# Kernel optimization log

Hardware: AMD Instinct MI355X
Metric: run time of the kernel (lower is better)

The kernel has to match this reference:

```python
import jax, jax.numpy as jnp
import numpy as np

# Static config (matches init_kwargs)
B, C, H, W = 16, 3, 64, 64
K = 32            # num_kernels
D = 5             # tree_depth
S = 1 << D        # leaves per tree = 32
R = 5             # receptive_field_size
STRIDE, PAD = 1, 0
TAU = 1.0
OH = (H + 2 * PAD - R) // STRIDE + 1
OW = (W + 2 * PAD - R) // STRIDE + 1
P = OH * OW       # number of output spatial positions

# LUT[op, t] = truth-table value of 2-input logic op `op` at minterm t = 2*a + b
LUT = jnp.asarray(np.array([[(op >> t) & 1 for t in range(4)]
                            for op in range(16)], dtype=np.float32))


def _combine(a, b, w):
    """Differentiable LUT node: softmax-weighted mixture of all 16 binary ops.
    a, b: (B, K, P, N) child activations; w: (N, K, 16) logits."""
    p = jax.nn.softmax(w / TAU, axis=-1)          # (N, K, 16)
    v = jnp.einsum('nko,ot->nkt', p, LUT)         # (N, K, 4) minterm coeffs
    c = jnp.transpose(v, (1, 0, 2))[None, :, None]  # (1, K, 1, N, 4)
    return (c[..., 0] * (1 - a) * (1 - b)
            + c[..., 1] * (1 - a) * b
            + c[..., 2] * a * (1 - b)
            + c[..., 3] * a * b)


def setup_inputs() -> dict:
    key = jax.random.key(0)
    ks = jax.random.split(key, 10)
    x = jax.random.uniform(ks[0], (B, C, H, W), dtype=jnp.float32)
    h_idx = jax.random.randint(ks[1], (2, K, S), 0, R, dtype=jnp.int32)
    w_idx = jax.random.randint(ks[2], (2, K, S), 0, R, dtype=jnp.int32)
    c_idx = jax.random.randint(ks[3], (2, K, S), 0, C, dtype=jnp.int32)
    node_counts = [S >> lvl for lvl in range(D + 1)]  # [32,16,8,4,2,1]
    ws = {f'w{i}': jax.random.normal(ks[4 + i], (n, K, 16), dtype=jnp.float32)
          for i, n in enumerate(node_counts)}
    return {'x': x, 'h_idx': h_idx, 'w_idx': w_idx, 'c_idx': c_idx, **ws}


def reference(x, h_idx, w_idx, c_idx, w0, w1, w2, w3, w4, w5):
    if PAD > 0:
        x = jnp.pad(x, ((0, 0), (0, 0), (PAD, PAD), (PAD, PAD)))
    # Absolute gather indices: leaf offsets + strided window origins
    off_h = jnp.repeat(jnp.arange(OH, dtype=jnp.int32) * STRIDE, OW)  # (P,)
    off_w = jnp.tile(jnp.arange(OW, dtype=jnp.int32) * STRIDE, OH)    # (P,)
    Habs = h_idx[:, :, None, :] + off_h[None, None, :, None]  # (2,K,P,S)
    Wabs = w_idx[:, :, None, :] + off_w[None, None, :, None]  # (2,K,P,S)
    Cabs = jnp.broadcast_to(c_idx[:, :, None, :], Habs.shape)  # (2,K,P,S)
    g = x[:, Cabs, Habs, Wabs]                                 # (B,2,K,P,S)

    # Level 0: combine the two gathered leaf inputs per node
    y = _combine(g[:, 0], g[:, 1], w0)                         # (B,K,P,S)
    # Levels 1..D: pair consecutive nodes and reduce up the binary tree
    for w in (w1, w2, w3, w4, w5):
        y = _combine(y[..., 0::2], y[..., 1::2], w)
    return y.reshape(y.shape[0], K, OH, OW)
```

## Files before the change

### kernel.cpp

```cpp
#include <hip/hip_runtime.h>
#include <hip/hip_fp16.h>
#include <math.h>

#define Bb   16
#define Cc   3
#define Hh   64
#define Ww   64
#define Kk   32
#define Ss   32
#define OHh  60
#define OWw  60
#define Pp   3600
#define ROWS 34
#define OHSUB 30
#define NGRP 450
#define TPB  256

#define DWROW  33
#define DWC    (ROWS * DWROW)
#define DWCOPY (Cc * DWC)

typedef float vf4 __attribute__((ext_vector_type(4)));
typedef float vf4u __attribute__((ext_vector_type(4), aligned(4)));

#define SB __builtin_amdgcn_sched_barrier(0)

static __device__ __forceinline__ vf4 vsplat(float s) { return (vf4){s, s, s, s}; }

static __device__ __forceinline__ vf4 comb(vf4 a, vf4 b, vf4 c) {
    const vf4 t = __builtin_elementwise_fma(b, vsplat(c.w), vsplat(c.y));
    const vf4 u = __builtin_elementwise_fma(b, vsplat(c.z), vsplat(c.x));
    return __builtin_elementwise_fma(a, t, u);
}

static __device__ __forceinline__ unsigned int pkh(float lo, float hi) {
    __half2 h = __floats2half2_rn(lo, hi);
    return *reinterpret_cast<unsigned int*>(&h);
}

#define GATH(dbase, dst)                                                     \
    {                                                                        \
        const unsigned int lo = xsh[(dbase) + loff];                         \
        const unsigned int hi = xsh[(dbase) + loff + 1];                     \
        const __half2 hl = *reinterpret_cast<const __half2*>(&lo);           \
        const __half2 hh = *reinterpret_cast<const __half2*>(&hi);           \
        const float2 fl = __half22float2(hl);                                \
        const float2 fh = __half22float2(hh);                                \
        dst = (vf4){fl.x, fl.y, fh.x, fh.y};                                 \
    }

#define STAGE(S, LASTQ, FOLD_DS, FOLD_FMA)                                    \
    vf4 t4_##S;                                                               \
    {                                                                         \
        vf4 A0, B0, A1, B1, A2, B2, A3, B3;                                   \
        GATH(cb0.x, A0); GATH(cb0.y, B0);                                     \
        GATH(cb1.x, A1); GATH(cb1.y, B1);                                     \
        GATH(cb2.x, A2); GATH(cb2.y, B2);                                     \
        GATH(cb3.x, A3); GATH(cb3.y, B3);                                     \
        const vf4 c0 = coefs[4*S], c1 = coefs[4*S+1];                         \
        const vf4 c2 = coefs[4*S+2], c3 = coefs[4*S+3];                       \
        const vf4 d0 = coefs[32+2*S], d1 = coefs[33+2*S], e0 = coefs[48+S];   \
        FOLD_DS                                                               \
        if constexpr (!(LASTQ)) {                                             \
            cb0 = bases[(4*S+4) & 31]; cb1 = bases[(4*S+5) & 31];             \
            cb2 = bases[(4*S+6) & 31]; cb3 = bases[(4*S+7) & 31];             \
        }                                                                     \
        const vf4 u0 = comb(A0, B0, c0), u1 = comb(A1, B1, c1);               \
        const vf4 u2 = comb(A2, B2, c2), u3 = comb(A3, B3, c3);               \
        t4_##S = comb(comb(u0, u1, d0), comb(u2, u3, d1), e0);                \
        FOLD_FMA                                                              \
        SB;                                                                   \
    }

__global__ __launch_bounds__(TPB) void logic_conv_kernel(
    const float* __restrict__ x,
    const int*   __restrict__ h_idx,
    const int*   __restrict__ w_idx,
    const int*   __restrict__ c_idx,
    const float* __restrict__ w0, const float* __restrict__ w1,
    const float* __restrict__ w2, const float* __restrict__ w3,
    const float* __restrict__ w4, const float* __restrict__ w5,
    float* __restrict__ out)
{
    __shared__ unsigned int xsh[2 * DWCOPY];
    __shared__ vf4  coefs[63];
    __shared__ int2 bases[32];

    const int tid  = threadIdx.x;
    const int blk  = blockIdx.x;
    const int b    = blk >> 6;
    const int k    = (blk >> 1) & 31;
    const int half = blk & 1;
    const int oh0  = half * OHSUB;

    const float* xb = x + b * (Cc * Hh * Ww);
    #pragma unroll
    for (int it = 0; it < 7; ++it) {
        const int flat = it * TPB + tid;
        if (flat < Cc * ROWS * 16) {
            const int c   = flat / (ROWS * 16);
            const int rem = flat - c * (ROWS * 16);
            const int r   = rem >> 4;
            const int w4i = rem & 15;
            const int w0c = w4i << 2;
            const float* src = xb + c * (Hh * Ww) + (oh0 + r) * Ww + w0c;
            const vf4u A = *reinterpret_cast<const vf4u*>(src);
            vf4u Bv;
            if (w4i < 15) Bv = *reinterpret_cast<const vf4u*>(src + 1);
            else          Bv = (vf4u){A.y, A.z, A.w, A.w};
            const int di = c * DWC + r * DWROW + (w0c >> 1);
            xsh[di]              = pkh(A.x, A.y);
            xsh[di + 1]          = pkh(A.z, A.w);
            xsh[DWCOPY + di]     = pkh(Bv.x, Bv.y);
            xsh[DWCOPY + di + 1] = pkh(Bv.z, Bv.w);
        }
    }

    if (tid < 32) {
        const int i0 = (0 * Kk + k) * Ss + tid;
        const int i1 = (1 * Kk + k) * Ss + tid;
        const int wA = w_idx[i0], sA = wA & 1;
        const int wB = w_idx[i1], sB = wB & 1;
        bases[tid] = make_int2(
            sA * DWCOPY + c_idx[i0] * DWC + h_idx[i0] * DWROW + ((wA - sA) >> 1),
            sB * DWCOPY + c_idx[i1] * DWC + h_idx[i1] * DWROW + ((wB - sB) >> 1));
    }

    if (tid >= 64 && tid < 127) {
        const int t = tid - 64;
        const float* wp; int n;
        if      (t < 32) { wp = w0; n = t;      }
        else if (t < 48) { wp = w1; n = t - 32; }
        else if (t < 56) { wp = w2; n = t - 48; }
        else if (t < 60) { wp = w3; n = t - 56; }
        else if (t < 62) { wp = w4; n = t - 60; }
        else             { wp = w5; n = 0;      }
        const float* lg = wp + (n * Kk + k) * 16;
        float l[16];
        float m = lg[0];
        #pragma unroll
        for (int q = 0; q < 16; ++q) { l[q] = lg[q]; m = fmaxf(m, l[q]); }
        float e[16], s = 0.f;
        #pragma unroll
        for (int q = 0; q < 16; ++q) { e[q] = __expf(l[q] - m); s += e[q]; }
        const float inv = 1.f / s;
        float c0 = 0.f, c1 = 0.f, c2 = 0.f, c3 = 0.f;
        #pragma unroll
        for (int op = 0; op < 16; ++op) {
            if (op & 1) c0 += e[op];
            if (op & 2) c1 += e[op];
            if (op & 4) c2 += e[op];
            if (op & 8) c3 += e[op];
        }
        c0 *= inv; c1 *= inv; c2 *= inv; c3 *= inv;
        coefs[t] = (vf4){c0, c2 - c0, c1 - c0, c0 - c1 - c2 + c3};
    }

    __syncthreads();

    float* outp = out + (b * Kk + k) * Pp + oh0 * OWw;
    #pragma unroll 1
    for (int it = 0; it < 2; ++it) {
        const int g = it * TPB + tid;
        if (g < NGRP) {
            const int oh   = g % OHSUB;
            const int owg  = g / OHSUB;
            const int loff = oh * DWROW + (owg << 1);

            int2 cb0 = bases[0], cb1 = bases[1], cb2 = bases[2], cb3 = bases[3];
            vf4 t8a, t8b, t16a, t16b, y;

            STAGE(0, 0, , )
            STAGE(1, 0,
                  const vf4 f0 = coefs[56];,
                  t8a = comb(t4_0, t4_1, f0);)
            STAGE(2, 0, , )
            STAGE(3, 0,
                  const vf4 f1 = coefs[57]; const vf4 g0 = coefs[60];,
                  t8b = comb(t4_2, t4_3, f1); t16a = comb(t8a, t8b, g0);)
            STAGE(4, 0, , )
            STAGE(5, 0,
                  const vf4 f2 = coefs[58];,
                  t8a = comb(t4_4, t4_5, f2);)
            STAGE(6, 0, , )
            STAGE(7, 1,
                  const vf4 f3 = coefs[59]; const vf4 g1 = coefs[61];
                  const vf4 rc = coefs[62];,
                  t8b = comb(t4_6, t4_7, f3); t16b = comb(t8a, t8b, g1);
                  y = comb(t16a, t16b, rc);)

            *reinterpret_cast<vf4*>(outp + oh * OWw + (owg << 2)) = y;
        }
    }
}

extern "C" void kernel_launch(void* const* d_in, const int* in_sizes, int n_in,
                              void* d_out, int out_size, void* d_ws, size_t ws_size,
                              hipStream_t stream) {
    const float* x     = (const float*)d_in[0];
    const int*   h_idx = (const int*)d_in[1];
    const int*   w_idx = (const int*)d_in[2];
    const int*   c_idx = (const int*)d_in[3];
    const float* w0    = (const float*)d_in[4];
    const float* w1    = (const float*)d_in[5];
    const float* w2    = (const float*)d_in[6];
    const float* w3    = (const float*)d_in[7];
    const float* w4    = (const float*)d_in[8];
    const float* w5    = (const float*)d_in[9];
    float* out = (float*)d_out;

    dim3 grid(Bb * Kk * 2);
    dim3 block(TPB);
    hipLaunchKernelGGL(logic_conv_kernel, grid, block, 0, stream,
                       x, h_idx, w_idx, c_idx, w0, w1, w2, w3, w4, w5, out);
}
```

Baseline: 22.23 us.

## Precompute coefficients in a separate kernel and split output into four strips

Moves the softmax coefficient and gather-base computation into a small pre-kernel that writes to workspace, so the main kernel no longer recomputes them once per (batch,k,half) block. The main kernel now reads the coefficients uniformly from global memory and splits each output map into four strips of 15 rows. That doubles the grid, removes the per-thread loop of two iterations, and shrinks shared memory per block. The cost is an extra kernel launch plus more redundant halo row loads of x across strips.

```diff
diff --git a/kernel.cpp b/kernel.cpp
--- a/kernel.cpp
+++ b/kernel.cpp
@@ -11,9 +11,9 @@
 #define OHh  60
 #define OWw  60
 #define Pp   3600
-#define ROWS 34
-#define OHSUB 30
-#define NGRP 450
+#define OHSUB 15
+#define ROWS 19
+#define NGRP 225
 #define TPB  256
 
 #define DWROW  33
@@ -38,96 +38,19 @@
     return *reinterpret_cast<unsigned int*>(&h);
 }
 
-#define GATH(dbase, dst)                                                     \
-    {                                                                        \
-        const unsigned int lo = xsh[(dbase) + loff];                         \
-        const unsigned int hi = xsh[(dbase) + loff + 1];                     \
-        const __half2 hl = *reinterpret_cast<const __half2*>(&lo);           \
-        const __half2 hh = *reinterpret_cast<const __half2*>(&hi);           \
-        const float2 fl = __half22float2(hl);                                \
-        const float2 fh = __half22float2(hh);                                \
-        dst = (vf4){fl.x, fl.y, fh.x, fh.y};                                 \
-    }
-
-#define STAGE(S, LASTQ, FOLD_DS, FOLD_FMA)                                    \
-    vf4 t4_##S;                                                               \
-    {                                                                         \
-        vf4 A0, B0, A1, B1, A2, B2, A3, B3;                                   \
-        GATH(cb0.x, A0); GATH(cb0.y, B0);                                     \
-        GATH(cb1.x, A1); GATH(cb1.y, B1);                                     \
-        GATH(cb2.x, A2); GATH(cb2.y, B2);                                     \
-        GATH(cb3.x, A3); GATH(cb3.y, B3);                                     \
-        const vf4 c0 = coefs[4*S], c1 = coefs[4*S+1];                         \
-        const vf4 c2 = coefs[4*S+2], c3 = coefs[4*S+3];                       \
-        const vf4 d0 = coefs[32+2*S], d1 = coefs[33+2*S], e0 = coefs[48+S];   \
-        FOLD_DS                                                               \
-        if constexpr (!(LASTQ)) {                                             \
-            cb0 = bases[(4*S+4) & 31]; cb1 = bases[(4*S+5) & 31];             \
-            cb2 = bases[(4*S+6) & 31]; cb3 = bases[(4*S+7) & 31];             \
-        }                                                                     \
-        const vf4 u0 = comb(A0, B0, c0), u1 = comb(A1, B1, c1);               \
-        const vf4 u2 = comb(A2, B2, c2), u3 = comb(A3, B3, c3);               \
-        t4_##S = comb(comb(u0, u1, d0), comb(u2, u3, d1), e0);                \
-        FOLD_FMA                                                              \
-        SB;                                                                   \
-    }
-
-__global__ __launch_bounds__(TPB) void logic_conv_kernel(
-    const float* __restrict__ x,
-    const int*   __restrict__ h_idx,
-    const int*   __restrict__ w_idx,
-    const int*   __restrict__ c_idx,
+__global__ __launch_bounds__(128) void coef_kernel(
+    const int* __restrict__ h_idx, const int* __restrict__ w_idx,
+    const int* __restrict__ c_idx,
     const float* __restrict__ w0, const float* __restrict__ w1,
     const float* __restrict__ w2, const float* __restrict__ w3,
     const float* __restrict__ w4, const float* __restrict__ w5,
-    float* __restrict__ out)
+    float* __restrict__ ws)
 {
-    __shared__ unsigned int xsh[2 * DWCOPY];
-    __shared__ vf4  coefs[63];
-    __shared__ int2 bases[32];
-
-    const int tid  = threadIdx.x;
-    const int blk  = blockIdx.x;
-    const int b    = blk >> 6;
-    const int k    = (blk >> 1) & 31;
-    const int half = blk & 1;
-    const int oh0  = half * OHSUB;
-
-    const float* xb = x + b * (Cc * Hh * Ww);
-    #pragma unroll
-    for (int it = 0; it < 7; ++it) {
-        const int flat = it * TPB + tid;
-        if (flat < Cc * ROWS * 16) {
-            const int c   = flat / (ROWS * 16);
-            const int rem = flat - c * (ROWS * 16);
-            const int r   = rem >> 4;
-            const int w4i = rem & 15;
-            const int w0c = w4i << 2;
-            const float* src = xb + c * (Hh * Ww) + (oh0 + r) * Ww + w0c;
-            const vf4u A = *reinterpret_cast<const vf4u*>(src);
-            vf4u Bv;
-            if (w4i < 15) Bv = *reinterpret_cast<const vf4u*>(src + 1);
-            else          Bv = (vf4u){A.y, A.z, A.w, A.w};
-            const int di = c * DWC + r * DWROW + (w0c >> 1);
-            xsh[di]              = pkh(A.x, A.y);
-            xsh[di + 1]          = pkh(A.z, A.w);
-            xsh[DWCOPY + di]     = pkh(Bv.x, Bv.y);
-            xsh[DWCOPY + di + 1] = pkh(Bv.z, Bv.w);
-        }
-    }
-
-    if (tid < 32) {
-        const int i0 = (0 * Kk + k) * Ss + tid;
-        const int i1 = (1 * Kk + k) * Ss + tid;
-        const int wA = w_idx[i0], sA = wA & 1;
-        const int wB = w_idx[i1], sB = wB & 1;
-        bases[tid] = make_int2(
-            sA * DWCOPY + c_idx[i0] * DWC + h_idx[i0] * DWROW + ((wA - sA) >> 1),
-            sB * DWCOPY + c_idx[i1] * DWC + h_idx[i1] * DWROW + ((wB - sB) >> 1));
-    }
-
-    if (tid >= 64 && tid < 127) {
-        const int t = tid - 64;
+    const int k = blockIdx.x;
+    const int t = threadIdx.x;
+    float* slot = ws + (k << 9);
+
+    if (t < 63) {
         const float* wp; int n;
         if      (t < 32) { wp = w0; n = t;      }
         else if (t < 48) { wp = w1; n = t - 32; }
@@ -153,44 +76,127 @@
             if (op & 8) c3 += e[op];
         }
         c0 *= inv; c1 *= inv; c2 *= inv; c3 *= inv;
-        coefs[t] = (vf4){c0, c2 - c0, c1 - c0, c0 - c1 - c2 + c3};
+        slot[t * 4 + 0] = c0;
+        slot[t * 4 + 1] = c2 - c0;
+        slot[t * 4 + 2] = c1 - c0;
+        slot[t * 4 + 3] = c0 - c1 - c2 + c3;
+    } else if (t >= 64 && t < 96) {
+        const int leaf = t - 64;
+        const int i0 = (0 * Kk + k) * Ss + leaf;
+        const int i1 = (1 * Kk + k) * Ss + leaf;
+        const int wA = w_idx[i0], sA = wA & 1;
+        const int wB = w_idx[i1], sB = wB & 1;
+        int2* bs = reinterpret_cast<int2*>(slot + 256);
+        bs[leaf] = make_int2(
+            sA * DWCOPY + c_idx[i0] * DWC + h_idx[i0] * DWROW + ((wA - sA) >> 1),
+            sB * DWCOPY + c_idx[i1] * DWC + h_idx[i1] * DWROW + ((wB - sB) >> 1));
+    }
+}
+
+#define GATH(sbase, dst)                                                     \
+    {                                                                        \
+        const unsigned int lo = xsh[(sbase) + loff];                         \
+        const unsigned int hi = xsh[(sbase) + loff + 1];                     \
+        const __half2 hl = *reinterpret_cast<const __half2*>(&lo);           \
+        const __half2 hh = *reinterpret_cast<const __half2*>(&hi);           \
+        const float2 fl = __half22float2(hl);                                \
+        const float2 fh = __half22float2(hh);                                \
+        dst = (vf4){fl.x, fl.y, fh.x, fh.y};                                 \
+    }
+
+#define LOADC(S)                                                              \
+    const vf4 c0_##S = ck[4*(S)],   c1_##S = ck[4*(S)+1];                     \
+    const vf4 c2_##S = ck[4*(S)+2], c3_##S = ck[4*(S)+3];                     \
+    const vf4 d0_##S = ck[32+2*(S)], d1_##S = ck[33+2*(S)];                   \
+    const vf4 e0_##S = ck[48+(S)];                                            \
+    const int2 b0_##S = bs[4*(S)],   b1_##S = bs[4*(S)+1];                    \
+    const int2 b2_##S = bs[4*(S)+2], b3_##S = bs[4*(S)+3];
+
+#define STAGE(S, FOLD)                                                        \
+    vf4 t4_##S;                                                               \
+    {                                                                         \
+        vf4 A0, B0, A1, B1, A2, B2, A3, B3;                                   \
+        GATH(b0_##S.x, A0); GATH(b0_##S.y, B0);                               \
+        GATH(b1_##S.x, A1); GATH(b1_##S.y, B1);                               \
+        GATH(b2_##S.x, A2); GATH(b2_##S.y, B2);                               \
+        GATH(b3_##S.x, A3); GATH(b3_##S.y, B3);                               \
+        const vf4 u0 = comb(A0, B0, c0_##S), u1 = comb(A1, B1, c1_##S);       \
+        const vf4 u2 = comb(A2, B2, c2_##S), u3 = comb(A3, B3, c3_##S);       \
+        t4_##S = comb(comb(u0, u1, d0_##S), comb(u2, u3, d1_##S), e0_##S);    \
+        FOLD                                                                  \
+        SB;                                                                   \
+    }
+
+__global__ __launch_bounds__(TPB) void logic_conv_kernel(
+    const float* __restrict__ x,
+    const float* __restrict__ cws,
+    float* __restrict__ out)
+{
+    __shared__ unsigned int xsh[2 * DWCOPY];
+
+    const int tid   = threadIdx.x;
+    const int blk   = blockIdx.x;
+    const int strip = blk & 3;
+    const int k     = __builtin_amdgcn_readfirstlane((blk >> 2) & 31);
+    const int b     = blk >> 7;
+    const int oh0   = strip * OHSUB;
+
+    const vf4*  ck = reinterpret_cast<const vf4*>(cws) + (k << 7);
+    const int2* bs = reinterpret_cast<const int2*>(ck + 64);
+
+    const float* xb = x + b * (Cc * Hh * Ww);
+    #pragma unroll
+    for (int it = 0; it < 4; ++it) {
+        const int flat = it * TPB + tid;
+        if (flat < Cc * ROWS * 16) {
+            const int c   = flat / (ROWS * 16);
+            const int rem = flat - c * (ROWS * 16);
+            const int r   = rem >> 4;
+            const int w4i = rem & 15;
+            const int w0c = w4i << 2;
+            const float* src = xb + c * (Hh * Ww) + (oh0 + r) * Ww + w0c;
+            const vf4u A = *reinterpret_cast<const vf4u*>(src);
+            vf4u Bv;
+            if (w4i < 15) Bv = *reinterpret_cast<const vf4u*>(src + 1);
+            else          Bv = (vf4u){A.y, A.z, A.w, A.w};
+            const int di = c * DWC + r * DWROW + (w0c >> 1);
+            xsh[di]              = pkh(A.x, A.y);
+            xsh[di + 1]          = pkh(A.z, A.w);
+            xsh[DWCOPY + di]     = pkh(Bv.x, Bv.y);
+            xsh[DWCOPY + di + 1] = pkh(Bv.z, Bv.w);
+        }
     }
 
     __syncthreads();
 
-    float* outp = out + (b * Kk + k) * Pp + oh0 * OWw;
-    #pragma unroll 1
-    for (int it = 0; it < 2; ++it) {
-        const int g = it * TPB + tid;
-        if (g < NGRP) {
-            const int oh   = g % OHSUB;
-            const int owg  = g / OHSUB;
-            const int loff = oh * DWROW + (owg << 1);
-
-            int2 cb0 = bases[0], cb1 = bases[1], cb2 = bases[2], cb3 = bases[3];
-            vf4 t8a, t8b, t16a, t16b, y;
-
-            STAGE(0, 0, , )
-            STAGE(1, 0,
-                  const vf4 f0 = coefs[56];,
-                  t8a = comb(t4_0, t4_1, f0);)
-            STAGE(2, 0, , )
-            STAGE(3, 0,
-                  const vf4 f1 = coefs[57]; const vf4 g0 = coefs[60];,
-                  t8b = comb(t4_2, t4_3, f1); t16a = comb(t8a, t8b, g0);)
-            STAGE(4, 0, , )
-            STAGE(5, 0,
-                  const vf4 f2 = coefs[58];,
-                  t8a = comb(t4_4, t4_5, f2);)
-            STAGE(6, 0, , )
-            STAGE(7, 1,
-                  const vf4 f3 = coefs[59]; const vf4 g1 = coefs[61];
-                  const vf4 rc = coefs[62];,
-                  t8b = comb(t4_6, t4_7, f3); t16b = comb(t8a, t8b, g1);
-                  y = comb(t16a, t16b, rc);)
-
-            *reinterpret_cast<vf4*>(outp + oh * OWw + (owg << 2)) = y;
-        }
+    if (tid < NGRP) {
+        const int oh   = tid % OHSUB;
+        const int owg  = tid / OHSUB;
+        const int loff = oh * DWROW + (owg << 1);
+
+        vf4 t8a, t8b, t16a, t16b, y;
+        LOADC(0)
+        LOADC(1)
+        STAGE(0, )
+        LOADC(2)
+        STAGE(1, t8a = comb(t4_0, t4_1, ck[56]);)
+        LOADC(3)
+        STAGE(2, )
+        LOADC(4)
+        STAGE(3, t8b = comb(t4_2, t4_3, ck[57]);
+                 t16a = comb(t8a, t8b, ck[60]);)
+        LOADC(5)
+        STAGE(4, )
+        LOADC(6)
+        STAGE(5, t8a = comb(t4_4, t4_5, ck[58]);)
+        LOADC(7)
+        STAGE(6, )
+        STAGE(7, t8b = comb(t4_6, t4_7, ck[59]);
+                 t16b = comb(t8a, t8b, ck[61]);
+                 y = comb(t16a, t16b, ck[62]);)
+
+        float* outp = out + (b * Kk + k) * Pp + (oh0 + oh) * OWw + (owg << 2);
+        *reinterpret_cast<vf4*>(outp) = y;
     }
 }
 
@@ -208,9 +214,13 @@
     const float* w4    = (const float*)d_in[8];
     const float* w5    = (const float*)d_in[9];
     float* out = (float*)d_out;
-
-    dim3 grid(Bb * Kk * 2);
+    float* cws = (float*)d_ws;
+
+    hipLaunchKernelGGL(coef_kernel, dim3(Kk), dim3(128), 0, stream,
+                       h_idx, w_idx, c_idx, w0, w1, w2, w3, w4, w5, cws);
+
+    dim3 grid(Bb * Kk * 4);
     dim3 block(TPB);
     hipLaunchKernelGGL(logic_conv_kernel, grid, block, 0, stream,
-                       x, h_idx, w_idx, c_idx, w0, w1, w2, w3, w4, w5, out);
-}
+                       x, cws, out);
+}
```

Result: slower. 26.88 us (+20.9%).

## Split output into four row strips per block and store input as fp32

Applied to the files above, without the earlier changes.

Each block now covers a 15-row strip instead of 30 rows, so the grid doubles and each thread processes one 4-wide group with no inner loop. The shared-memory input copy stays fp32 (two shifted copies) rather than being packed into fp16, which removes the convert work in the gather and the fp16 rounding. In exchange, more rows are re-staged per output because of the halo, the coefficient softmax and index setup run in twice as many blocks, and shared memory per block grows relative to the rows it holds.

```diff
diff --git a/kernel.cpp b/kernel.cpp
--- a/kernel.cpp
+++ b/kernel.cpp
@@ -1,5 +1,4 @@
 #include <hip/hip_runtime.h>
-#include <hip/hip_fp16.h>
 #include <math.h>
 
 #define Bb   16
@@ -11,14 +10,14 @@
 #define OHh  60
 #define OWw  60
 #define Pp   3600
-#define ROWS 34
-#define OHSUB 30
-#define NGRP 450
+#define OHSUB 15
+#define ROWS 19
+#define NGRP 225
 #define TPB  256
 
-#define DWROW  33
-#define DWC    (ROWS * DWROW)
-#define DWCOPY (Cc * DWC)
+#define FROW  66
+#define FCH   (ROWS * FROW)
+#define FCOPY (Cc * FCH)
 
 typedef float vf4 __attribute__((ext_vector_type(4)));
 typedef float vf4u __attribute__((ext_vector_type(4), aligned(4)));
@@ -33,23 +32,14 @@
     return __builtin_elementwise_fma(a, t, u);
 }
 
-static __device__ __forceinline__ unsigned int pkh(float lo, float hi) {
-    __half2 h = __floats2half2_rn(lo, hi);
-    return *reinterpret_cast<unsigned int*>(&h);
-}
-
-#define GATH(dbase, dst)                                                     \
+#define GATH(fbase, dst)                                                     \
     {                                                                        \
-        const unsigned int lo = xsh[(dbase) + loff];                         \
-        const unsigned int hi = xsh[(dbase) + loff + 1];                     \
-        const __half2 hl = *reinterpret_cast<const __half2*>(&lo);           \
-        const __half2 hh = *reinterpret_cast<const __half2*>(&hi);           \
-        const float2 fl = __half22float2(hl);                                \
-        const float2 fh = __half22float2(hh);                                \
-        dst = (vf4){fl.x, fl.y, fh.x, fh.y};                                 \
+        const float2 lo = *reinterpret_cast<const float2*>(&xsh[(fbase) + loff]);     \
+        const float2 hi = *reinterpret_cast<const float2*>(&xsh[(fbase) + loff + 2]); \
+        dst = (vf4){lo.x, lo.y, hi.x, hi.y};                                 \
     }
 
-#define STAGE(S, LASTQ, FOLD_DS, FOLD_FMA)                                    \
+#define STAGE(S, LASTQ, FOLD)                                                 \
     vf4 t4_##S;                                                               \
     {                                                                         \
         vf4 A0, B0, A1, B1, A2, B2, A3, B3;                                   \
@@ -60,7 +50,6 @@
         const vf4 c0 = coefs[4*S], c1 = coefs[4*S+1];                         \
         const vf4 c2 = coefs[4*S+2], c3 = coefs[4*S+3];                       \
         const vf4 d0 = coefs[32+2*S], d1 = coefs[33+2*S], e0 = coefs[48+S];   \
-        FOLD_DS                                                               \
         if constexpr (!(LASTQ)) {                                             \
             cb0 = bases[(4*S+4) & 31]; cb1 = bases[(4*S+5) & 31];             \
             cb2 = bases[(4*S+6) & 31]; cb3 = bases[(4*S+7) & 31];             \
@@ -68,7 +57,7 @@
         const vf4 u0 = comb(A0, B0, c0), u1 = comb(A1, B1, c1);               \
         const vf4 u2 = comb(A2, B2, c2), u3 = comb(A3, B3, c3);               \
         t4_##S = comb(comb(u0, u1, d0), comb(u2, u3, d1), e0);                \
-        FOLD_FMA                                                              \
+        FOLD                                                                  \
         SB;                                                                   \
     }
 
@@ -82,37 +71,36 @@
     const float* __restrict__ w4, const float* __restrict__ w5,
     float* __restrict__ out)
 {
-    __shared__ unsigned int xsh[2 * DWCOPY];
-    __shared__ vf4  coefs[63];
-    __shared__ int2 bases[32];
+    __shared__ float xsh[2 * FCOPY];
+    __shared__ vf4   coefs[63];
+    __shared__ int2  bases[32];
 
-    const int tid  = threadIdx.x;
-    const int blk  = blockIdx.x;
-    const int b    = blk >> 6;
-    const int k    = (blk >> 1) & 31;
-    const int half = blk & 1;
-    const int oh0  = half * OHSUB;
+    const int tid   = threadIdx.x;
+    const int blk   = blockIdx.x;
+    const int k     = blk & 31;
+    const int strip = (blk >> 5) & 3;
+    const int b     = blk >> 7;
+    const int oh0   = strip * OHSUB;
 
     const float* xb = x + b * (Cc * Hh * Ww);
     #pragma unroll
-    for (int it = 0; it < 7; ++it) {
+    for (int it = 0; it < 4; ++it) {
         const int flat = it * TPB + tid;
         if (flat < Cc * ROWS * 16) {
             const int c   = flat / (ROWS * 16);
             const int rem = flat - c * (ROWS * 16);
             const int r   = rem >> 4;
-            const int w4i = rem & 15;
-            const int w0c = w4i << 2;
-            const float* src = xb + c * (Hh * Ww) + (oh0 + r) * Ww + w0c;
+            const int j   = rem & 15;
+            const float* src = xb + c * (Hh * Ww) + (oh0 + r) * Ww + (j << 2);
             const vf4u A = *reinterpret_cast<const vf4u*>(src);
             vf4u Bv;
-            if (w4i < 15) Bv = *reinterpret_cast<const vf4u*>(src + 1);
-            else          Bv = (vf4u){A.y, A.z, A.w, A.w};
-            const int di = c * DWC + r * DWROW + (w0c >> 1);
-            xsh[di]              = pkh(A.x, A.y);
-            xsh[di + 1]          = pkh(A.z, A.w);
-            xsh[DWCOPY + di]     = pkh(Bv.x, Bv.y);
-            xsh[DWCOPY + di + 1] = pkh(Bv.z, Bv.w);
+            if (j < 15) Bv = *reinterpret_cast<const vf4u*>(src + 1);
+            else        Bv = (vf4u){A.y, A.z, A.w, A.w};
+            const int di = c * FCH + r * FROW + (j << 2);
+            *reinterpret_cast<float2*>(&xsh[di])              = make_float2(A.x, A.y);
+            *reinterpret_cast<float2*>(&xsh[di + 2])          = make_float2(A.z, A.w);
+            *reinterpret_cast<float2*>(&xsh[FCOPY + di])      = make_float2(Bv.x, Bv.y);
+            *reinterpret_cast<float2*>(&xsh[FCOPY + di + 2])  = make_float2(Bv.z, Bv.w);
         }
     }
 
@@ -122,8 +110,8 @@
         const int wA = w_idx[i0], sA = wA & 1;
         const int wB = w_idx[i1], sB = wB & 1;
         bases[tid] = make_int2(
-            sA * DWCOPY + c_idx[i0] * DWC + h_idx[i0] * DWROW + ((wA - sA) >> 1),
-            sB * DWCOPY + c_idx[i1] * DWC + h_idx[i1] * DWROW + ((wB - sB) >> 1));
+            sA * FCOPY + c_idx[i0] * FCH + h_idx[i0] * FROW + (wA - sA),
+            sB * FCOPY + c_idx[i1] * FCH + h_idx[i1] * FROW + (wB - sB));
     }
 
     if (tid >= 64 && tid < 127) {
@@ -158,39 +146,28 @@
 
     __syncthreads();
 
-    float* outp = out + (b * Kk + k) * Pp + oh0 * OWw;
-    #pragma unroll 1
-    for (int it = 0; it < 2; ++it) {
-        const int g = it * TPB + tid;
-        if (g < NGRP) {
-            const int oh   = g % OHSUB;
-            const int owg  = g / OHSUB;
-            const int loff = oh * DWROW + (owg << 1);
+    if (tid < NGRP) {
+        const int oh   = tid % OHSUB;
+        const int owg  = tid / OHSUB;
+        const int loff = oh * FROW + (owg << 2);
 
-            int2 cb0 = bases[0], cb1 = bases[1], cb2 = bases[2], cb3 = bases[3];
-            vf4 t8a, t8b, t16a, t16b, y;
+        int2 cb0 = bases[0], cb1 = bases[1], cb2 = bases[2], cb3 = bases[3];
+        vf4 t8a, t8b, t16a, t16b, y;
 
-            STAGE(0, 0, , )
-            STAGE(1, 0,
-                  const vf4 f0 = coefs[56];,
-                  t8a = comb(t4_0, t4_1, f0);)
-            STAGE(2, 0, , )
-            STAGE(3, 0,
-                  const vf4 f1 = coefs[57]; const vf4 g0 = coefs[60];,
-                  t8b = comb(t4_2, t4_3, f1); t16a = comb(t8a, t8b, g0);)
-            STAGE(4, 0, , )
-            STAGE(5, 0,
-                  const vf4 f2 = coefs[58];,
-                  t8a = comb(t4_4, t4_5, f2);)
-            STAGE(6, 0, , )
-            STAGE(7, 1,
-                  const vf4 f3 = coefs[59]; const vf4 g1 = coefs[61];
-                  const vf4 rc = coefs[62];,
-                  t8b = comb(t4_6, t4_7, f3); t16b = comb(t8a, t8b, g1);
-                  y = comb(t16a, t16b, rc);)
+        STAGE(0, 0, )
+        STAGE(1, 0, t8a = comb(t4_0, t4_1, coefs[56]);)
+        STAGE(2, 0, )
+        STAGE(3, 0, t8b = comb(t4_2, t4_3, coefs[57]);
+                    t16a = comb(t8a, t8b, coefs[60]);)
+        STAGE(4, 0, )
+        STAGE(5, 0, t8a = comb(t4_4, t4_5, coefs[58]);)
+        STAGE(6, 0, )
+        STAGE(7, 1, t8b = comb(t4_6, t4_7, coefs[59]);
+                    t16b = comb(t8a, t8b, coefs[61]);
+                    y = comb(t16a, t16b, coefs[62]);)
 
-            *reinterpret_cast<vf4*>(outp + oh * OWw + (owg << 2)) = y;
-        }
+        float* outp = out + (b * Kk + k) * Pp + (oh0 + oh) * OWw + (owg << 2);
+        *reinterpret_cast<vf4*>(outp) = y;
     }
 }
 
@@ -209,7 +186,7 @@
     const float* w5    = (const float*)d_in[9];
     float* out = (float*)d_out;
 
-    dim3 grid(Bb * Kk * 2);
+    dim3 grid(Bb * Kk * 4);
     dim3 block(TPB);
     hipLaunchKernelGGL(logic_conv_kernel, grid, block, 0, stream,
                        x, h_idx, w_idx, c_idx, w0, w1, w2, w3, w4, w5, out);
```

Measured after the change: 33.74 us. +51.8%, slower.
